# Kernel optimization log

Hardware: AMD Instinct MI355X
Metric: run time of the kernel (lower is better)

## Reference

```python
import jax, jax.numpy as jnp
import numpy as np

# Fixed molemap hierarchy: leaf groups under level-2 nodes 65..72
GROUPS = [(0, 7), (7, 30), (30, 48), (48, 53), (53, 58), (58, 59), (59, 62), (62, 65)]
GROUP_SIZES = [b - a for a, b in GROUPS]
# group index of each leaf (which of nodes 65..72 is its parent)
GIDX = np.repeat(np.arange(8), GROUP_SIZES)
# top branch of each leaf: 0 -> node 73 (leaves 0..52), 1 -> node 74 (leaves 53..64)
TIDX = (np.arange(65) >= 53).astype(np.int32)


def _forward(x):
    # x: [N, 65] leaf logits
    N = x.shape[0]
    # leaf-level probs: softmax of leaf logits within each sibling group (children of 65..72)
    leaf_probs = jnp.concatenate(
        [jax.nn.softmax(x[:, a:b], axis=-1) for a, b in GROUPS], axis=-1
    )  # [N, 65]
    # level-2 node logits = mean of their leaf logits (nodes 65..72)
    means = jnp.stack([x[:, a:b].mean(axis=-1) for a, b in GROUPS], axis=-1)  # [N, 8]
    # level-1 node logits = mean over all leaves beneath (node 73: leaves 0..52, node 74: 53..64)
    m_top = jnp.stack([x[:, :53].mean(axis=-1), x[:, 53:].mean(axis=-1)], axis=-1)  # [N, 2]
    p_top = jax.nn.softmax(m_top, axis=-1)  # [N, 2] -> nodes 73, 74
    # level-2 probs: softmax among siblings (65..68 under 73, 69..72 under 74)
    p_lvl2 = jnp.concatenate(
        [jax.nn.softmax(means[:, :4], axis=-1), jax.nn.softmax(means[:, 4:], axis=-1)],
        axis=-1,
    )  # [N, 8] -> nodes 65..72
    # node_probs layout: [leaves 0..64 | nodes 65..72 | nodes 73..74 | root 75 (=1)]
    node_probs = jnp.concatenate(
        [leaf_probs, p_lvl2, p_top, jnp.ones((N, 1), dtype=x.dtype)], axis=-1
    )  # [N, 76]
    # root-to-leaf path product: p(root)=1 * p(level1) * p(level2) * p(leaf)
    leaf_path_probs = leaf_probs * p_lvl2[:, GIDX] * p_top[:, TIDX]  # [N, 65]
    return leaf_path_probs, node_probs


def setup_inputs() -> dict:
    key = jax.random.key(0)
    x = jax.random.normal(key, (524288, 65), dtype=jnp.float32)
    return {"x": x}


def reference(x):
    return _forward(x)
```

## Files before the change

### kernel.cpp

```cpp
#include <hip/hip_runtime.h>
#include <math.h>


#define NLEAF 65
#define NNODE 76
#define ROWS  64
#define TPB   64

#define NF4    ((ROWS * NLEAF) / 4)
#define NQ4    ((ROWS * NNODE) / 4)
#define FULL_A (NF4 / TPB)
#define TAIL_A (NF4 - FULL_A * TPB)
#define FULL_E (NQ4 / TPB)

__device__ __forceinline__ void async_copy16(const float4* g, float4* l) {
    __builtin_amdgcn_global_load_lds(
        (const __attribute__((address_space(1))) void*)g,
        (__attribute__((address_space(3))) void*)l,
        16, 0, 0);
}

__global__ __launch_bounds__(TPB, 2) void hier_molemap_kernel(
    const float* __restrict__ x,
    float* __restrict__ out_leaf,
    float* __restrict__ out_node,
    int N)
{
    __shared__ float lds[ROWS * NNODE];

    const int tid  = threadIdx.x;
    const int row0 = blockIdx.x * ROWS;
    if (row0 >= N) return;
    const int R    = min(ROWS, N - row0);
    const bool full = (R == ROWS);

    if (full) {
        const float4* __restrict__ src4 = (const float4*)(x + (size_t)row0 * NLEAF);
        float4* lds4 = (float4*)lds;
#pragma unroll
        for (int i = 0; i < FULL_A; ++i)
            async_copy16(src4 + tid + i * TPB, lds4 + tid + i * TPB);
        if (tid < TAIL_A)
            async_copy16(src4 + tid + FULL_A * TPB, lds4 + tid + FULL_A * TPB);
    } else {
        const float* __restrict__ src = x + (size_t)row0 * NLEAF;
        for (int i = tid; i < R * NLEAF; i += TPB) lds[i] = src[i];
    }
    __syncthreads();

    float v[NLEAF];
    float p2[8];
    float pt0 = 0.0f, pt1 = 0.0f;

    constexpr int ga[8] = {0, 7, 30, 48, 53, 58, 59, 62};
    constexpr int gb[8] = {7, 30, 48, 53, 58, 59, 62, 65};

    if (tid < R) {
        const float* __restrict__ r = lds + tid * NLEAF;
#pragma unroll
        for (int i = 0; i < NLEAF; ++i) v[i] = r[i];

        float gsum[8], means[8];
#pragma unroll
        for (int g = 0; g < 8; ++g) {
            float mx = -INFINITY, sx = 0.0f;
#pragma unroll
            for (int i = ga[g]; i < gb[g]; ++i) { mx = fmaxf(mx, v[i]); sx += v[i]; }
            gsum[g]  = sx;
            means[g] = sx * (1.0f / (float)(gb[g] - ga[g]));
            float denom = 0.0f;
#pragma unroll
            for (int i = ga[g]; i < gb[g]; ++i) {
                float e = __expf(v[i] - mx);
                v[i] = e;
                denom += e;
            }
            float inv = 1.0f / denom;
#pragma unroll
            for (int i = ga[g]; i < gb[g]; ++i) v[i] *= inv;
        }

        float m0 = (gsum[0] + gsum[1] + gsum[2] + gsum[3]) * (1.0f / 53.0f);
        float m1 = (gsum[4] + gsum[5] + gsum[6] + gsum[7]) * (1.0f / 12.0f);
        float mt = fmaxf(m0, m1);
        float e0 = __expf(m0 - mt), e1 = __expf(m1 - mt);
        float invt = 1.0f / (e0 + e1);
        pt0 = e0 * invt; pt1 = e1 * invt;

        float mxa = fmaxf(fmaxf(means[0], means[1]), fmaxf(means[2], means[3]));
        float sa = 0.0f;
#pragma unroll
        for (int g = 0; g < 4; ++g) { p2[g] = __expf(means[g] - mxa); sa += p2[g]; }
        float inva = 1.0f / sa;
#pragma unroll
        for (int g = 0; g < 4; ++g) p2[g] *= inva;

        float mxb = fmaxf(fmaxf(means[4], means[5]), fmaxf(means[6], means[7]));
        float sb = 0.0f;
#pragma unroll
        for (int g = 4; g < 8; ++g) { p2[g] = __expf(means[g] - mxb); sb += p2[g]; }
        float invb = 1.0f / sb;
#pragma unroll
        for (int g = 4; g < 8; ++g) p2[g] *= invb;

        float* __restrict__ w = lds + tid * NLEAF;
#pragma unroll
        for (int g = 0; g < 8; ++g) {
            float f = p2[g] * ((g < 4) ? pt0 : pt1);
#pragma unroll
            for (int i = ga[g]; i < gb[g]; ++i) w[i] = v[i] * f;
        }
    }
    asm volatile("s_waitcnt lgkmcnt(0)" ::: "memory");

    if (full) {
        float4* __restrict__ dst4 = (float4*)(out_leaf + (size_t)row0 * NLEAF);
        const float4* lds4 = (const float4*)lds;
#pragma unroll
        for (int i = 0; i < FULL_A; ++i) {
            int idx = tid + i * TPB;
            dst4[idx] = lds4[idx];
        }
        if (tid < TAIL_A) {
            int idx = tid + FULL_A * TPB;
            dst4[idx] = lds4[idx];
        }
    } else {
        float* __restrict__ dst = out_leaf + (size_t)row0 * NLEAF;
        for (int i = tid; i < R * NLEAF; i += TPB) dst[i] = lds[i];
    }
    asm volatile("s_waitcnt lgkmcnt(0)" ::: "memory");

    if (tid < R) {
        float4* __restrict__ nrow4 = (float4*)lds + tid * (NNODE / 4);
#pragma unroll
        for (int c = 0; c < 16; ++c) {
            float4 t;
            t.x = v[4 * c + 0];
            t.y = v[4 * c + 1];
            t.z = v[4 * c + 2];
            t.w = v[4 * c + 3];
            nrow4[c] = t;
        }
        float4 t16; t16.x = v[64];  t16.y = p2[0]; t16.z = p2[1]; t16.w = p2[2];
        nrow4[16] = t16;
        float4 t17; t17.x = p2[3];  t17.y = p2[4]; t17.z = p2[5]; t17.w = p2[6];
        nrow4[17] = t17;
        float4 t18; t18.x = p2[7];  t18.y = pt0;   t18.z = pt1;   t18.w = 1.0f;
        nrow4[18] = t18;
    }
    asm volatile("s_waitcnt lgkmcnt(0)" ::: "memory");

    if (full) {
        float4* __restrict__ dst4 = (float4*)(out_node + (size_t)row0 * NNODE);
        const float4* lds4 = (const float4*)lds;
#pragma unroll
        for (int i = 0; i < FULL_E; ++i) {
            int q = tid + i * TPB;
            dst4[q] = lds4[q];
        }
    } else {
        float* __restrict__ dst = out_node + (size_t)row0 * NNODE;
        for (int j = tid; j < R * NNODE; j += TPB) dst[j] = lds[j];
    }
}

extern "C" void kernel_launch(void* const* d_in, const int* in_sizes, int n_in,
                              void* d_out, int out_size, void* d_ws, size_t ws_size,
                              hipStream_t stream) {
    const float* x = (const float*)d_in[0];
    int N = in_sizes[0] / NLEAF;

    float* out_leaf = (float*)d_out;
    float* out_node = (float*)d_out + (size_t)N * NLEAF;

    int grid = (N + ROWS - 1) / ROWS;
    hier_molemap_kernel<<<grid, TPB, 0, stream>>>(x, out_leaf, out_node, N);
}
```

Before: 386.3 us.

## Persistent blocks with double-buffered async LDS prefetch and nontemporal stores

Switches to a persistent grid of at most 2048 blocks. Each block processes a contiguous run of 32-row batches and prefetches the next batch into a second LDS buffer with global_load_lds while the current one is computed, waiting with a partial vmcnt. Output stores use nontemporal hints. Only half the threads do row work per batch, and the hand-set vmcnt count is fragile. With 2048 blocks of one wave each, latency hiding may be limited.

```diff
diff --git a/kernel.cpp b/kernel.cpp
--- a/kernel.cpp
+++ b/kernel.cpp
@@ -4,20 +4,86 @@
 
 #define NLEAF 65
 #define NNODE 76
-#define ROWS  64
+#define ROWS  32
 #define TPB   64
-
-#define NF4    ((ROWS * NLEAF) / 4)
-#define NQ4    ((ROWS * NNODE) / 4)
-#define FULL_A (NF4 / TPB)
-#define TAIL_A (NF4 - FULL_A * TPB)
-#define FULL_E (NQ4 / TPB)
+#define GRIDMAX 2048
+
+#define IN_F4   ((ROWS * NLEAF) / 4)
+#define IN_FULL (IN_F4 / TPB)
+#define IN_TAIL (IN_F4 - IN_FULL * TPB)
+#define ND_F4   ((ROWS * NNODE) / 4)
+#define ND_FULL (ND_F4 / TPB)
+#define ND_TAIL (ND_F4 - ND_FULL * TPB)
+#define BUFW    (ROWS * NNODE)
+
+typedef float f32x4 __attribute__((ext_vector_type(4)));
 
 __device__ __forceinline__ void async_copy16(const float4* g, float4* l) {
     __builtin_amdgcn_global_load_lds(
         (const __attribute__((address_space(1))) void*)g,
         (__attribute__((address_space(3))) void*)l,
         16, 0, 0);
+}
+
+__device__ __forceinline__ void dma_batch(const float* __restrict__ x,
+                                          size_t r0, float* buf, int tid) {
+    const float4* __restrict__ src4 = (const float4*)(x + r0 * NLEAF);
+    float4* d4 = (float4*)buf;
+#pragma unroll
+    for (int i = 0; i < IN_FULL; ++i)
+        async_copy16(src4 + tid + i * TPB, d4 + tid + i * TPB);
+    if (tid < IN_TAIL)
+        async_copy16(src4 + tid + IN_FULL * TPB, d4 + tid + IN_FULL * TPB);
+}
+
+__device__ __forceinline__ void row_softmax(float* __restrict__ v,
+                                            float* __restrict__ p2,
+                                            float& pt0, float& pt1) {
+    constexpr int ga[8] = {0, 7, 30, 48, 53, 58, 59, 62};
+    constexpr int gb[8] = {7, 30, 48, 53, 58, 59, 62, 65};
+
+    float gsum[8], means[8];
+#pragma unroll
+    for (int g = 0; g < 8; ++g) {
+        float mx = -INFINITY, sx = 0.0f;
+#pragma unroll
+        for (int i = ga[g]; i < gb[g]; ++i) { mx = fmaxf(mx, v[i]); sx += v[i]; }
+        gsum[g]  = sx;
+        means[g] = sx * (1.0f / (float)(gb[g] - ga[g]));
+        float denom = 0.0f;
+#pragma unroll
+        for (int i = ga[g]; i < gb[g]; ++i) {
+            float e = __expf(v[i] - mx);
+            v[i] = e;
+            denom += e;
+        }
+        float inv = 1.0f / denom;
+#pragma unroll
+        for (int i = ga[g]; i < gb[g]; ++i) v[i] *= inv;
+    }
+
+    float m0 = (gsum[0] + gsum[1] + gsum[2] + gsum[3]) * (1.0f / 53.0f);
+    float m1 = (gsum[4] + gsum[5] + gsum[6] + gsum[7]) * (1.0f / 12.0f);
+    float mt = fmaxf(m0, m1);
+    float e0 = __expf(m0 - mt), e1 = __expf(m1 - mt);
+    float invt = 1.0f / (e0 + e1);
+    pt0 = e0 * invt; pt1 = e1 * invt;
+
+    float mxa = fmaxf(fmaxf(means[0], means[1]), fmaxf(means[2], means[3]));
+    float sa = 0.0f;
+#pragma unroll
+    for (int g = 0; g < 4; ++g) { p2[g] = __expf(means[g] - mxa); sa += p2[g]; }
+    float inva = 1.0f / sa;
+#pragma unroll
+    for (int g = 0; g < 4; ++g) p2[g] *= inva;
+
+    float mxb = fmaxf(fmaxf(means[4], means[5]), fmaxf(means[6], means[7]));
+    float sb = 0.0f;
+#pragma unroll
+    for (int g = 4; g < 8; ++g) { p2[g] = __expf(means[g] - mxb); sb += p2[g]; }
+    float invb = 1.0f / sb;
+#pragma unroll
+    for (int g = 4; g < 8; ++g) p2[g] *= invb;
 }
 
 __global__ __launch_bounds__(TPB, 2) void hier_molemap_kernel(
@@ -26,142 +92,137 @@
     float* __restrict__ out_node,
     int N)
 {
-    __shared__ float lds[ROWS * NNODE];
-
-    const int tid  = threadIdx.x;
-    const int row0 = blockIdx.x * ROWS;
-    if (row0 >= N) return;
-    const int R    = min(ROWS, N - row0);
-    const bool full = (R == ROWS);
-
-    if (full) {
-        const float4* __restrict__ src4 = (const float4*)(x + (size_t)row0 * NLEAF);
-        float4* lds4 = (float4*)lds;
-#pragma unroll
-        for (int i = 0; i < FULL_A; ++i)
-            async_copy16(src4 + tid + i * TPB, lds4 + tid + i * TPB);
-        if (tid < TAIL_A)
-            async_copy16(src4 + tid + FULL_A * TPB, lds4 + tid + FULL_A * TPB);
-    } else {
-        const float* __restrict__ src = x + (size_t)row0 * NLEAF;
-        for (int i = tid; i < R * NLEAF; i += TPB) lds[i] = src[i];
-    }
-    __syncthreads();
-
-    float v[NLEAF];
-    float p2[8];
-    float pt0 = 0.0f, pt1 = 0.0f;
+    __shared__ float lds[2][BUFW];
+    const int tid = threadIdx.x;
+
+    const int nbatch  = (N + ROWS - 1) / ROWS;
+    const int nblocks = (int)gridDim.x;
+    const int per = (nbatch + nblocks - 1) / nblocks;
+    const int b0  = blockIdx.x * per;
+    const int b1  = min(nbatch, b0 + per);
+    if (b0 >= b1) return;
+
+    float* cur = lds[0];
+    float* nxt = lds[1];
 
     constexpr int ga[8] = {0, 7, 30, 48, 53, 58, 59, 62};
     constexpr int gb[8] = {7, 30, 48, 53, 58, 59, 62, 65};
 
-    if (tid < R) {
-        const float* __restrict__ r = lds + tid * NLEAF;
-#pragma unroll
-        for (int i = 0; i < NLEAF; ++i) v[i] = r[i];
-
-        float gsum[8], means[8];
-#pragma unroll
-        for (int g = 0; g < 8; ++g) {
-            float mx = -INFINITY, sx = 0.0f;
-#pragma unroll
-            for (int i = ga[g]; i < gb[g]; ++i) { mx = fmaxf(mx, v[i]); sx += v[i]; }
-            gsum[g]  = sx;
-            means[g] = sx * (1.0f / (float)(gb[g] - ga[g]));
-            float denom = 0.0f;
-#pragma unroll
-            for (int i = ga[g]; i < gb[g]; ++i) {
-                float e = __expf(v[i] - mx);
-                v[i] = e;
-                denom += e;
-            }
-            float inv = 1.0f / denom;
-#pragma unroll
-            for (int i = ga[g]; i < gb[g]; ++i) v[i] *= inv;
+    if (N - b0 * ROWS >= ROWS)
+        dma_batch(x, (size_t)b0 * ROWS, cur, tid);
+
+    for (int b = b0; b < b1; ++b) {
+        const size_t r0 = (size_t)b * ROWS;
+        const bool full      = ((size_t)N - r0 >= ROWS);
+        const bool next_full = (b + 1 < b1) && ((size_t)N - (r0 + ROWS) >= ROWS);
+
+        if (next_full) {
+            asm volatile("" ::: "memory");
+            dma_batch(x, r0 + ROWS, nxt, tid);
         }
 
-        float m0 = (gsum[0] + gsum[1] + gsum[2] + gsum[3]) * (1.0f / 53.0f);
-        float m1 = (gsum[4] + gsum[5] + gsum[6] + gsum[7]) * (1.0f / 12.0f);
-        float mt = fmaxf(m0, m1);
-        float e0 = __expf(m0 - mt), e1 = __expf(m1 - mt);
-        float invt = 1.0f / (e0 + e1);
-        pt0 = e0 * invt; pt1 = e1 * invt;
-
-        float mxa = fmaxf(fmaxf(means[0], means[1]), fmaxf(means[2], means[3]));
-        float sa = 0.0f;
-#pragma unroll
-        for (int g = 0; g < 4; ++g) { p2[g] = __expf(means[g] - mxa); sa += p2[g]; }
-        float inva = 1.0f / sa;
-#pragma unroll
-        for (int g = 0; g < 4; ++g) p2[g] *= inva;
-
-        float mxb = fmaxf(fmaxf(means[4], means[5]), fmaxf(means[6], means[7]));
-        float sb = 0.0f;
-#pragma unroll
-        for (int g = 4; g < 8; ++g) { p2[g] = __expf(means[g] - mxb); sb += p2[g]; }
-        float invb = 1.0f / sb;
-#pragma unroll
-        for (int g = 4; g < 8; ++g) p2[g] *= invb;
-
-        float* __restrict__ w = lds + tid * NLEAF;
-#pragma unroll
-        for (int g = 0; g < 8; ++g) {
-            float f = p2[g] * ((g < 4) ? pt0 : pt1);
-#pragma unroll
-            for (int i = ga[g]; i < gb[g]; ++i) w[i] = v[i] * f;
+        if (full) {
+            if (next_full) asm volatile("s_waitcnt vmcnt(9)" ::: "memory");
+            else           asm volatile("s_waitcnt vmcnt(0)" ::: "memory");
+
+            float v[NLEAF];
+            float p2[8];
+            float pt0 = 0.0f, pt1 = 0.0f;
+
+            if (tid < ROWS) {
+                const float* __restrict__ r = cur + tid * NLEAF;
+#pragma unroll
+                for (int i = 0; i < NLEAF; ++i) v[i] = r[i];
+
+                row_softmax(v, p2, pt0, pt1);
+
+                float* __restrict__ w = cur + tid * NLEAF;
+#pragma unroll
+                for (int g = 0; g < 8; ++g) {
+                    float f = p2[g] * ((g < 4) ? pt0 : pt1);
+#pragma unroll
+                    for (int i = ga[g]; i < gb[g]; ++i) w[i] = v[i] * f;
+                }
+            }
+            asm volatile("s_waitcnt lgkmcnt(0)" ::: "memory");
+
+            {
+                f32x4* __restrict__ dst4 = (f32x4*)(out_leaf + r0 * NLEAF);
+                const f32x4* s4 = (const f32x4*)cur;
+#pragma unroll
+                for (int i = 0; i < IN_FULL; ++i) {
+                    int q = tid + i * TPB;
+                    __builtin_nontemporal_store(s4[q], dst4 + q);
+                }
+                if (tid < IN_TAIL) {
+                    int q = tid + IN_FULL * TPB;
+                    __builtin_nontemporal_store(s4[q], dst4 + q);
+                }
+            }
+            asm volatile("" ::: "memory");
+
+            if (tid < ROWS) {
+                float4* __restrict__ nrow4 = (float4*)cur + tid * (NNODE / 4);
+#pragma unroll
+                for (int c = 0; c < 16; ++c) {
+                    float4 t;
+                    t.x = v[4 * c + 0];
+                    t.y = v[4 * c + 1];
+                    t.z = v[4 * c + 2];
+                    t.w = v[4 * c + 3];
+                    nrow4[c] = t;
+                }
+                float4 t16; t16.x = v[64];  t16.y = p2[0]; t16.z = p2[1]; t16.w = p2[2];
+                nrow4[16] = t16;
+                float4 t17; t17.x = p2[3];  t17.y = p2[4]; t17.z = p2[5]; t17.w = p2[6];
+                nrow4[17] = t17;
+                float4 t18; t18.x = p2[7];  t18.y = pt0;   t18.z = pt1;   t18.w = 1.0f;
+                nrow4[18] = t18;
+            }
+            asm volatile("s_waitcnt lgkmcnt(0)" ::: "memory");
+
+            {
+                f32x4* __restrict__ dst4 = (f32x4*)(out_node + r0 * NNODE);
+                const f32x4* s4 = (const f32x4*)cur;
+#pragma unroll
+                for (int i = 0; i < ND_FULL; ++i) {
+                    int q = tid + i * TPB;
+                    __builtin_nontemporal_store(s4[q], dst4 + q);
+                }
+                if (tid < ND_TAIL) {
+                    int q = tid + ND_FULL * TPB;
+                    __builtin_nontemporal_store(s4[q], dst4 + q);
+                }
+            }
+        } else {
+            const int R = (int)((size_t)N - r0);
+            if (tid < R) {
+                float v[NLEAF];
+                float p2[8];
+                float pt0, pt1;
+                const float* __restrict__ src = x + (r0 + tid) * NLEAF;
+#pragma unroll
+                for (int i = 0; i < NLEAF; ++i) v[i] = src[i];
+                row_softmax(v, p2, pt0, pt1);
+                float* __restrict__ dl = out_leaf + (r0 + tid) * NLEAF;
+                float* __restrict__ dn = out_node + (r0 + tid) * NNODE;
+#pragma unroll
+                for (int g = 0; g < 8; ++g) {
+                    float f = p2[g] * ((g < 4) ? pt0 : pt1);
+#pragma unroll
+                    for (int i = ga[g]; i < gb[g]; ++i) dl[i] = v[i] * f;
+                }
+#pragma unroll
+                for (int i = 0; i < NLEAF; ++i) dn[i] = v[i];
+#pragma unroll
+                for (int g = 0; g < 8; ++g) dn[NLEAF + g] = p2[g];
+                dn[73] = pt0;
+                dn[74] = pt1;
+                dn[75] = 1.0f;
+            }
         }
-    }
-    asm volatile("s_waitcnt lgkmcnt(0)" ::: "memory");
-
-    if (full) {
-        float4* __restrict__ dst4 = (float4*)(out_leaf + (size_t)row0 * NLEAF);
-        const float4* lds4 = (const float4*)lds;
-#pragma unroll
-        for (int i = 0; i < FULL_A; ++i) {
-            int idx = tid + i * TPB;
-            dst4[idx] = lds4[idx];
-        }
-        if (tid < TAIL_A) {
-            int idx = tid + FULL_A * TPB;
-            dst4[idx] = lds4[idx];
-        }
-    } else {
-        float* __restrict__ dst = out_leaf + (size_t)row0 * NLEAF;
-        for (int i = tid; i < R * NLEAF; i += TPB) dst[i] = lds[i];
-    }
-    asm volatile("s_waitcnt lgkmcnt(0)" ::: "memory");
-
-    if (tid < R) {
-        float4* __restrict__ nrow4 = (float4*)lds + tid * (NNODE / 4);
-#pragma unroll
-        for (int c = 0; c < 16; ++c) {
-            float4 t;
-            t.x = v[4 * c + 0];
-            t.y = v[4 * c + 1];
-            t.z = v[4 * c + 2];
-            t.w = v[4 * c + 3];
-            nrow4[c] = t;
-        }
-        float4 t16; t16.x = v[64];  t16.y = p2[0]; t16.z = p2[1]; t16.w = p2[2];
-        nrow4[16] = t16;
-        float4 t17; t17.x = p2[3];  t17.y = p2[4]; t17.z = p2[5]; t17.w = p2[6];
-        nrow4[17] = t17;
-        float4 t18; t18.x = p2[7];  t18.y = pt0;   t18.z = pt1;   t18.w = 1.0f;
-        nrow4[18] = t18;
-    }
-    asm volatile("s_waitcnt lgkmcnt(0)" ::: "memory");
-
-    if (full) {
-        float4* __restrict__ dst4 = (float4*)(out_node + (size_t)row0 * NNODE);
-        const float4* lds4 = (const float4*)lds;
-#pragma unroll
-        for (int i = 0; i < FULL_E; ++i) {
-            int q = tid + i * TPB;
-            dst4[q] = lds4[q];
-        }
-    } else {
-        float* __restrict__ dst = out_node + (size_t)row0 * NNODE;
-        for (int j = tid; j < R * NNODE; j += TPB) dst[j] = lds[j];
+
+        float* t = cur; cur = nxt; nxt = t;
     }
 }
 
@@ -174,6 +235,7 @@
     float* out_leaf = (float*)d_out;
     float* out_node = (float*)d_out + (size_t)N * NLEAF;
 
-    int grid = (N + ROWS - 1) / ROWS;
+    int nbatch = (N + ROWS - 1) / ROWS;
+    int grid   = nbatch < GRIDMAX ? nbatch : GRIDMAX;
     hier_molemap_kernel<<<grid, TPB, 0, stream>>>(x, out_leaf, out_node, N);
 }
```

Result: slower. 403.6 us (+4.5%).
